# Kernel tuning notes

Hardware: AMD Instinct MI355X
Metric: run time of the kernel (lower is better)

## Reference

```python
import jax, jax.numpy as jnp
import numpy as np

NUM_LABELS = 32
EMB = 128          # label_embedding_dim
HID = 1024         # hidden_dim (== encoder feature dim)
B, S = 128, 512


def setup_inputs() -> dict:
    key = jax.random.key(0)
    ks = jax.random.split(key, 8)
    k = 1.0 / np.sqrt(HID)  # torch GRU/Linear default init bound
    u = lambda kk, shape: jax.random.uniform(kk, shape, jnp.float32, minval=-k, maxval=k)
    return {
        "hidden_states": jax.random.normal(ks[0], (B, S, HID), jnp.float32),
        "emb": jax.random.normal(ks[1], (NUM_LABELS, EMB), jnp.float32),  # nn.Embedding ~ N(0,1)
        "W_ih": u(ks[2], (3 * HID, EMB + HID)),  # GRU input weights, gate order r,z,n
        "W_hh": u(ks[3], (3 * HID, HID)),
        "b_ih": u(ks[4], (3 * HID,)),
        "b_hh": u(ks[5], (3 * HID,)),
        "W_out": u(ks[6], (NUM_LABELS, HID)),
        "b_out": u(ks[7], (NUM_LABELS,)),
    }


def reference(hidden_states, emb, W_ih, W_hh, b_ih, b_hh, W_out, b_out):
    batch = hidden_states.shape[0]
    h0 = jnp.zeros((batch, W_hh.shape[1]), hidden_states.dtype)
    lab0 = jnp.broadcast_to(emb[0], (batch, emb.shape[1]))  # label_start_embedding (id 0)

    def step(carry, x_t):
        h, lab = carry
        inp = jnp.concatenate([x_t, lab], axis=-1)            # [B, HID+EMB]
        gi = inp @ W_ih.T + b_ih                               # [B, 3*HID]
        gh = h @ W_hh.T + b_hh
        ir, iz, in_ = jnp.split(gi, 3, axis=-1)
        hr, hz, hn = jnp.split(gh, 3, axis=-1)
        r = jax.nn.sigmoid(ir + hr)
        z = jax.nn.sigmoid(iz + hz)
        n = jnp.tanh(in_ + r * hn)
        h_new = (1.0 - z) * n + z * h                          # PyTorch GRU update
        logit = h_new @ W_out.T + b_out                        # dropout is identity in eval
        pred = jnp.argmax(logit, axis=-1)                      # softmax is monotone; argmax(probs)==argmax(logit)
        return (h_new, emb[pred]), logit

    xs = jnp.swapaxes(hidden_states, 0, 1)                     # [S, B, HID]
    _, logits = jax.lax.scan(step, (h0, lab0), xs)             # logits: [S, B, L]
    return jnp.swapaxes(logits, 0, 1)                          # [B, S, L]
```

## Files before the change

### kernel.cpp

```cpp
#include <hip/hip_runtime.h>


#define S_    512
#define HID_  1024
#define EMB_  128
#define NL_   32
#define G3_   3072

#define LDS_A_STRIDE 1032
#define LDS_A_BYTES  (48 * LDS_A_STRIDE * 2)
#define CP_STRIDE    52
#define LDS_CP_BYTES (4 * 64 * CP_STRIDE * 4)
#define LDS_BYTES    (LDS_A_BYTES + LDS_CP_BYTES)

typedef __attribute__((ext_vector_type(8))) short          short8;
typedef __attribute__((ext_vector_type(8))) unsigned short u16x8;
typedef __attribute__((ext_vector_type(4))) unsigned short u16x4;
typedef __attribute__((ext_vector_type(4))) float          f32x4;
typedef unsigned long long u64_t;

__device__ unsigned int   g_ctr[576];
__device__ unsigned int   g_flag[1];
__device__ unsigned int   g_vis[256];
__device__ unsigned int   g_predflag;
__device__ int            g_pred[128];
__device__ unsigned short g_hhi[2][128 * HID_];
__device__ unsigned short g_hlo[2][128 * HID_];
__device__ float          g_hf32[2][128 * HID_];
__device__ float          g_Glab[NL_ * G3_];
__device__ unsigned short g_Wlox[G3_ * HID_];
__device__ unsigned short g_Wlohh[G3_ * HID_];
__device__ float          g_GIXall[(size_t)S_ * 128 * 64 * 48];

__device__ __forceinline__ float bf2f(unsigned short u) {
  union { unsigned int i; float f; } v; v.i = ((unsigned int)u) << 16; return v.f;
}
__device__ __forceinline__ unsigned short f2bf(float f) {
  union { float f; unsigned int i; } v; v.f = f;
  unsigned int u = v.i;
  return (unsigned short)((u + 0x7FFFu + ((u >> 16) & 1u)) >> 16);
}
__device__ __forceinline__ short8 ld_bf8(const unsigned short* p) {
  return __builtin_bit_cast(short8, *(const u16x8*)p);
}
__device__ __forceinline__ float ldin(const void* p, long i, int f32) {
  return f32 ? ((const float*)p)[i] : bf2f(((const unsigned short*)p)[i]);
}
__device__ __forceinline__ void store_out(void* out, int f32, long idx, float v) {
  if (f32) ((float*)out)[idx] = v;
  else     ((unsigned short*)out)[idx] = f2bf(v);
}

__device__ __forceinline__ u64_t ald64(const void* p) {
  return __hip_atomic_load((const u64_t*)p, __ATOMIC_RELAXED,
                           __HIP_MEMORY_SCOPE_AGENT);
}
__device__ __forceinline__ void ast64(void* p, u64_t v) {
  __hip_atomic_store((u64_t*)p, v, __ATOMIC_RELAXED,
                     __HIP_MEMORY_SCOPE_AGENT);
}
__device__ __forceinline__ unsigned int ald32(const unsigned int* p) {
  return __hip_atomic_load(p, __ATOMIC_RELAXED, __HIP_MEMORY_SCOPE_AGENT);
}
__device__ __forceinline__ void ast32(unsigned int* p, unsigned int v) {
  __hip_atomic_store(p, v, __ATOMIC_RELAXED, __HIP_MEMORY_SCOPE_AGENT);
}
__device__ __forceinline__ int aldi(const int* p) {
  return __hip_atomic_load(p, __ATOMIC_RELAXED, __HIP_MEMORY_SCOPE_AGENT);
}
__device__ __forceinline__ void asti(int* p, int v) {
  __hip_atomic_store(p, v, __ATOMIC_RELAXED, __HIP_MEMORY_SCOPE_AGENT);
}
__device__ __forceinline__ short8 ld_bf8_coh(const unsigned short* p) {
  union { u64_t q[2]; short8 s; } u;
  u.q[0] = ald64(p);
  u.q[1] = ald64(p + 4);
  return u.s;
}
__device__ __forceinline__ f32x4 ld_f4_coh(const float* p) {
  union { u64_t q[2]; f32x4 f; } u;
  u.q[0] = ald64(p);
  u.q[1] = ald64(p + 2);
  return u.f;
}
__device__ __forceinline__ void st_f4_coh(float* p, f32x4 v) {
  union { f32x4 f; u64_t q[2]; } u; u.f = v;
  ast64(p, u.q[0]);
  ast64(p + 2, u.q[1]);
}
__device__ __forceinline__ void st_h4_coh(unsigned short* p, u16x4 v) {
  union { u16x4 h; u64_t q; } u; u.h = v;
  ast64(p, u.q);
}

__global__ void k_zero() {
  int t = blockIdx.x * 256 + threadIdx.x;
  if (t < 576) g_ctr[t] = 0u;
  else if (t < 832) g_vis[t - 576] = 0u;
  else if (t < 960) g_pred[t - 832] = 0;
  else if (t == 960) g_predflag = 0u;
  const u16x4 z4 = {0, 0, 0, 0};
  const f32x4 zf = {0.f, 0.f, 0.f, 0.f};
  for (int i = t; i < 2 * 128 * HID_ / 4; i += 65536) {
    ((u16x4*)g_hhi)[i] = z4;
    ((u16x4*)g_hlo)[i] = z4;
    ((f32x4*)g_hf32)[i] = zf;
  }
}

__global__ void k_detect(const unsigned short* __restrict__ W) {
  unsigned bad = 0;
  for (int i = threadIdx.x; i < 1024; i += 64) {
    float v = bf2f(W[i]);
    if (!(v * v <= 1.0f)) bad = 1;
  }
  unsigned long long b = __ballot(bad != 0);
  if (threadIdx.x == 0) g_flag[0] = (b != 0ull) ? 1u : 0u;
}

__global__ void k_prep(const void* __restrict__ emb,
                       const void* __restrict__ W_ih,
                       const void* __restrict__ b_ih) {
  const int f32 = (int)g_flag[0];
  int l = blockIdx.x / 12;
  int n = (blockIdx.x % 12) * 256 + threadIdx.x;
  double acc = (double)ldin(b_ih, n, f32);
  for (int e = 0; e < EMB_; ++e)
    acc += (double)ldin(emb, (long)l * EMB_ + e, f32) *
           (double)ldin(W_ih, (long)n * (HID_ + EMB_) + HID_ + e, f32);
  g_Glab[l * G3_ + n] = (float)acc;
}

__global__ void k_prepw(const void* __restrict__ W_ih,
                        const void* __restrict__ W_hh) {
  if (!g_flag[0]) return;
  long i4 = ((long)blockIdx.x * 256 + threadIdx.x) * 4;
  if (i4 >= (long)G3_ * HID_) return;
  int row = (int)(i4 >> 10), col = (int)(i4 & 1023);
  f32x4 wh = *(const f32x4*)&((const float*)W_hh)[(long)row * HID_ + col];
  f32x4 wx = *(const f32x4*)&((const float*)W_ih)[(long)row * (HID_ + EMB_) + col];
  u16x4 lh, lx;
  #pragma unroll
  for (int j = 0; j < 4; ++j) {
    unsigned short h1 = f2bf(wh[j]);
    lh[j] = f2bf(wh[j] - bf2f(h1));
    unsigned short x1 = f2bf(wx[j]);
    lx[j] = f2bf(wx[j] - bf2f(x1));
  }
  *(u16x4*)&g_Wlohh[i4] = lh;
  *(u16x4*)&g_Wlox[i4]  = lx;
}

__device__ __forceinline__ void gridbar(int wg, int bar) {
  __syncthreads();
  if (threadIdx.x == 0) {
    asm volatile("s_waitcnt vmcnt(0)" ::: "memory");
    unsigned int* c1   = g_ctr + (wg & 7) * 64;
    unsigned int* root = g_ctr + 512;
    unsigned int old = __hip_atomic_fetch_add(c1, 1u, __ATOMIC_RELAXED,
                                              __HIP_MEMORY_SCOPE_AGENT);
    if (old == 32u * (unsigned)(bar + 1) - 1u)
      __hip_atomic_fetch_add(root, 1u, __ATOMIC_RELAXED,
                             __HIP_MEMORY_SCOPE_AGENT);
    unsigned int tgt = 8u * (unsigned)(bar + 1);
    while (__hip_atomic_load(root, __ATOMIC_RELAXED,
                             __HIP_MEMORY_SCOPE_AGENT) < tgt)
      __builtin_amdgcn_s_sleep(1);
  }
  __syncthreads();
}

__device__ __forceinline__ void stage_w(unsigned short* sA, const void* Wsrc,
                                        int wstride, int rg, int f32, int tid) {
  if (f32) {
    const float* Ws = (const float*)Wsrc;
    for (int i = tid; i < 48 * 1024 / 4; i += 256) {
      int e = i * 4, row = e >> 10, k4 = e & 1023;
      int grow = (row >> 4) * HID_ + rg * 16 + (row & 15);
      f32x4 v = *(const f32x4*)&Ws[(long)grow * wstride + k4];
      u16x4 o;
      #pragma unroll
      for (int j = 0; j < 4; ++j) o[j] = f2bf(v[j]);
      *(u16x4*)&sA[row * LDS_A_STRIDE + k4] = o;
    }
  } else {
    const unsigned short* Ws = (const unsigned short*)Wsrc;
    for (int i = tid; i < 48 * 1024 / 4; i += 256) {
      int e = i * 4, row = e >> 10, k4 = e & 1023;
      int grow = (row >> 4) * HID_ + rg * 16 + (row & 15);
      *(u16x4*)&sA[row * LDS_A_STRIDE + k4] =
          *(const u16x4*)&Ws[(long)grow * wstride + k4];
    }
  }
}

__global__ __launch_bounds__(256) void k_seq(
    const void* __restrict__ hs,
    const void* __restrict__ W_ih,
    const void* __restrict__ W_hh,
    const void* __restrict__ b_hh,
    const void* __restrict__ W_out,
    const void* __restrict__ b_out,
    void* __restrict__ out) {
  extern __shared__ char smem[];
  unsigned short* sA  = (unsigned short*)smem;
  float*          sCp = (float*)(smem + LDS_A_BYTES);

  const int f32 = (int)g_flag[0];
  const int tid = threadIdx.x;
  const int wg  = blockIdx.x;
  const bool isx = (wg < 128);
  const int lid  = isx ? wg : wg - 128;
  const int rg = lid >> 1, bg = lid & 1;
  const int slot = lid;
  const int lane = tid & 63, wv = tid >> 6;
  const int m = lane & 15, q = lane >> 4;
  const int bl = tid & 63;
  const int jj = (tid >> 6) * 4;
  const int kw0 = wv * 256 + q * 8;

  int bar = 0;

  if (tid == 0) ast32(&g_vis[wg], (unsigned)wg + 1u);
  gridbar(wg, bar); ++bar;
  if (tid == 0) {
    unsigned p = ((unsigned)wg + 37u) & 255u;
    if (ald32(&g_vis[p]) != p + 1u) store_out(out, f32, wg, 999.0f);
  }

  {
    const int slot0 = wg & 127;
    const int rg0 = slot0 >> 1, bg0 = slot0 & 1;
    stage_w(sA, W_ih, HID_ + EMB_, rg0, f32, tid);
    __syncthreads();
    const long bstride = (long)S_ * HID_;
    const long boffb = (long)(bg0 * 64) * S_ * HID_;
    for (int t = 0; t < 256; ++t) {
      const int it = ((wg >> 7) << 8) | t;
      f32x4 acc[3][4];
      #pragma unroll
      for (int rt = 0; rt < 3; ++rt)
        #pragma unroll
        for (int bt = 0; bt < 4; ++bt) acc[rt][bt] = f32x4{0.f, 0.f, 0.f, 0.f};
      const long boff = boffb + (long)it * HID_;
      if (f32) {
        const float* Bf = (const float*)hs + boff;
        #pragma unroll
        for (int kb = 0; kb < 8; ++kb) {
          const int k = kw0 + kb * 32;
          short8 avh[3];
          #pragma unroll
          for (int rt = 0; rt < 3; ++rt)
            avh[rt] = ld_bf8(&sA[(rt * 16 + m) * LDS_A_STRIDE + k]);
          short8 bxh[4], bxl[4];
          #pragma unroll
          for (int bt = 0; bt < 4; ++bt) {
            const float* bp = Bf + (long)(bt * 16 + m) * bstride + k;
            f32x4 x0 = *(const f32x4*)bp;
            f32x4 x1 = *(const f32x4*)(bp + 4);
            u16x8 th, tl;
            #pragma unroll
            for (int j = 0; j < 4; ++j) {
              unsigned short u0 = f2bf(x0[j]);
              th[j] = u0; tl[j] = f2bf(x0[j] - bf2f(u0));
              unsigned short u1 = f2bf(x1[j]);
              th[4 + j] = u1; tl[4 + j] = f2bf(x1[j] - bf2f(u1));
            }
            bxh[bt] = __builtin_bit_cast(short8, th);
            bxl[bt] = __builtin_bit_cast(short8, tl);
          }
          short8 avl[3];
          #pragma unroll
          for (int rt = 0; rt < 3; ++rt)
            avl[rt] = ld_bf8(&g_Wlox[(long)(rt * HID_ + rg0 * 16 + m) * HID_ + k]);
          #pragma unroll
          for (int rt = 0; rt < 3; ++rt)
            #pragma unroll
            for (int bt = 0; bt < 4; ++bt) {
              acc[rt][bt] = __builtin_amdgcn_mfma_f32_16x16x32_bf16(
                  avh[rt], bxh[bt], acc[rt][bt], 0, 0, 0);
              acc[rt][bt] = __builtin_amdgcn_mfma_f32_16x16x32_bf16(
                  avh[rt], bxl[bt], acc[rt][bt], 0, 0, 0);
              acc[rt][bt] = __builtin_amdgcn_mfma_f32_16x16x32_bf16(
                  avl[rt], bxh[bt], acc[rt][bt], 0, 0, 0);
              acc[rt][bt] = __builtin_amdgcn_mfma_f32_16x16x32_bf16(
                  avl[rt], bxl[bt], acc[rt][bt], 0, 0, 0);
            }
        }
      } else {
        const unsigned short* Bh = (const unsigned short*)hs + boff;
        #pragma unroll
        for (int kb = 0; kb < 8; ++kb) {
          const int k = kw0 + kb * 32;
          short8 avh[3], bxh[4];
          #pragma unroll
          for (int rt = 0; rt < 3; ++rt)
            avh[rt] = ld_bf8(&sA[(rt * 16 + m) * LDS_A_STRIDE + k]);
          #pragma unroll
          for (int bt = 0; bt < 4; ++bt)
            bxh[bt] = ld_bf8(&Bh[(long)(bt * 16 + m) * bstride + k]);
          #pragma unroll
          for (int rt = 0; rt < 3; ++rt)
            #pragma unroll
            for (int bt = 0; bt < 4; ++bt)
              acc[rt][bt] = __builtin_amdgcn_mfma_f32_16x16x32_bf16(
                  avh[rt], bxh[bt], acc[rt][bt], 0, 0, 0);
        }
      }
      __syncthreads();
      #pragma unroll
      for (int rt = 0; rt < 3; ++rt)
        #pragma unroll
        for (int bt = 0; bt < 4; ++bt)
          *(f32x4*)&sCp[(wv * 64 + bt * 16 + m) * CP_STRIDE + rt * 16 + q * 4] =
              acc[rt][bt];
      __syncthreads();
      #pragma unroll
      for (int g = 0; g < 3; ++g) {
        f32x4 sv = f32x4{0.f, 0.f, 0.f, 0.f};
        #pragma unroll
        for (int w = 0; w < 4; ++w)
          sv += *(const f32x4*)&sCp[(w * 64 + bl) * CP_STRIDE + g * 16 + jj];
        *(f32x4*)&g_GIXall[(((long)it * 128 + slot0) * 64 + bl) * 48 +
                           g * 16 + jj] = sv;
      }
      __syncthreads();
    }
  }
  __threadfence();
  gridbar(wg, bar); ++bar;

  if (!isx) stage_w(sA, W_hh, HID_, rg, f32, tid);
  __syncthreads();

  float bo = 0.f;
  if (isx && tid < 32) bo = ldin(b_out, tid, f32);
  f32x4 bhh[3];
  if (!isx) {
    const int jbase = rg * 16 + jj;
    #pragma unroll
    for (int g = 0; g < 3; ++g)
      #pragma unroll
      for (int t = 0; t < 4; ++t)
        bhh[g][t] = ldin(b_hh, (long)g * HID_ + jbase + t, f32);
  }

  float hreg[4] = {0.f, 0.f, 0.f, 0.f};
  f32x4 sred[3];

  for (int it = 0; it <= S_; ++it) {
    gridbar(wg, bar); ++bar;

    if (isx && it >= 1) {
      const int rb = (it + 1) & 1;
      if (it == 1 && wg == 0 && tid == 0) {
        float s = 0.f;
        for (int i = 0; i < 16; ++i) {
          union { u64_t q; float f[2]; } u; u.q = ald64(&g_hf32[0][2 * i]);
          s += u.f[0] * u.f[0] + u.f[1] * u.f[1];
        }
        if (s == 0.f) store_out(out, f32, 300, 555.0f);
      }
      const int b = wg, s = it - 1;
      float* scrp  = sCp;
      float* shrow = sCp + 256;
      {
        f32x4 hv = ld_f4_coh(&g_hf32[rb][(long)b * HID_ + tid * 4]);
        *(f32x4*)&shrow[(tid >> 5) * 132 + (tid & 31) * 4] = hv;
      }
      __syncthreads();
      {
        int l = tid >> 3, kc = tid & 7;
        const float* hr = shrow + kc * 132;
        float p = 0.f;
        if (f32) {
          const float* wr = (const float*)W_out + (long)l * HID_ + kc * 128;
          for (int k = 0; k < 128; k += 4) {
            f32x4 wa = *(const f32x4*)&wr[k];
            f32x4 ha = *(const f32x4*)&hr[k];
            #pragma unroll
            for (int j = 0; j < 4; ++j) p += wa[j] * ha[j];
          }
        } else {
          const unsigned short* wr =
              (const unsigned short*)W_out + (long)l * HID_ + kc * 128;
          for (int k = 0; k < 128; k += 8) {
            u16x8 w8 = *(const u16x8*)&wr[k];
            f32x4 ha = *(const f32x4*)&hr[k];
            f32x4 hb = *(const f32x4*)&hr[k + 4];
            #pragma unroll
            for (int j = 0; j < 4; ++j) {
              p += bf2f(w8[j]) * ha[j];
              p += bf2f(w8[4 + j]) * hb[j];
            }
          }
        }
        scrp[tid] = p;
      }
      __syncthreads();
      if (tid < 32) {
        const float* pp = sCp + tid * 8;
        float v = pp[0] + pp[1] + pp[2] + pp[3] + pp[4] + pp[5] + pp[6] + pp[7]
                  + bo;
        store_out(out, f32, ((long)b * S_ + s) * NL_ + tid, v);
        float bv = v; int bi = tid;
        #pragma unroll
        for (int off = 16; off; off >>= 1) {
          float v2 = __shfl_down(bv, off, 32);
          int   i2 = __shfl_down(bi, off, 32);
          if (v2 > bv || (v2 == bv && i2 < bi)) { bv = v2; bi = i2; }
        }
        if (tid == 0) {
          asti(&g_pred[b], bi);
          asm volatile("s_waitcnt vmcnt(0)" ::: "memory");
          __hip_atomic_fetch_add(&g_predflag, 1u, __ATOMIC_RELAXED,
                                 __HIP_MEMORY_SCOPE_AGENT);
        }
      }
      __syncthreads();
    }

    if (!isx && it < S_) {
      const int rb = (it + 1) & 1;
      const int wb = it & 1;
      f32x4 gixp[3];
      #pragma unroll
      for (int g = 0; g < 3; ++g)
        gixp[g] = *(const f32x4*)&g_GIXall[(((long)it * 128 + slot) * 64 + bl)
                                           * 48 + g * 16 + jj];

      f32x4 acc[3][4];
      #pragma unroll
      for (int rt = 0; rt < 3; ++rt)
        #pragma unroll
        for (int bt = 0; bt < 4; ++bt) acc[rt][bt] = f32x4{0.f, 0.f, 0.f, 0.f};

      const unsigned short* Bhi = g_hhi[rb] + (long)(bg * 64) * HID_;
      const unsigned short* Blo = g_hlo[rb] + (long)(bg * 64) * HID_;
      #pragma unroll
      for (int kb = 0; kb < 8; ++kb) {
        const int k = kw0 + kb * 32;
        short8 avh[3], bh[4], blv[4];
        #pragma unroll
        for (int rt = 0; rt < 3; ++rt)
          avh[rt] = ld_bf8(&sA[(rt * 16 + m) * LDS_A_STRIDE + k]);
        #pragma unroll
        for (int bt = 0; bt < 4; ++bt) {
          bh[bt]  = ld_bf8_coh(&Bhi[(long)(bt * 16 + m) * HID_ + k]);
          blv[bt] = ld_bf8_coh(&Blo[(long)(bt * 16 + m) * HID_ + k]);
        }
        #pragma unroll
        for (int rt = 0; rt < 3; ++rt)
          #pragma unroll
          for (int bt = 0; bt < 4; ++bt) {
            acc[rt][bt] = __builtin_amdgcn_mfma_f32_16x16x32_bf16(
                avh[rt], bh[bt], acc[rt][bt], 0, 0, 0);
            acc[rt][bt] = __builtin_amdgcn_mfma_f32_16x16x32_bf16(
                avh[rt], blv[bt], acc[rt][bt], 0, 0, 0);
          }
        if (f32) {
          short8 avl[3];
          #pragma unroll
          for (int rt = 0; rt < 3; ++rt)
            avl[rt] = ld_bf8(&g_Wlohh[(long)(rt * HID_ + rg * 16 + m) * HID_ + k]);
          #pragma unroll
          for (int rt = 0; rt < 3; ++rt)
            #pragma unroll
            for (int bt = 0; bt < 4; ++bt) {
              acc[rt][bt] = __builtin_amdgcn_mfma_f32_16x16x32_bf16(
                  avl[rt], bh[bt], acc[rt][bt], 0, 0, 0);
              acc[rt][bt] = __builtin_amdgcn_mfma_f32_16x16x32_bf16(
                  avl[rt], blv[bt], acc[rt][bt], 0, 0, 0);
            }
        }
      }

      __syncthreads();
      #pragma unroll
      for (int rt = 0; rt < 3; ++rt)
        #pragma unroll
        for (int bt = 0; bt < 4; ++bt)
          *(f32x4*)&sCp[(wv * 64 + bt * 16 + m) * CP_STRIDE + rt * 16 + q * 4] =
              acc[rt][bt];
      __syncthreads();
      #pragma unroll
      for (int g = 0; g < 3; ++g) {
        f32x4 sv = f32x4{0.f, 0.f, 0.f, 0.f};
        #pragma unroll
        for (int w = 0; w < 4; ++w)
          sv += *(const f32x4*)&sCp[(w * 64 + bl) * CP_STRIDE + g * 16 + jj];
        sred[g] = sv;
      }

      if (it >= 1) {
        if (tid == 0) {
          unsigned tgt = 128u * (unsigned)it;
          while (ald32(&g_predflag) < tgt) __builtin_amdgcn_s_sleep(1);
        }
        __syncthreads();
      }

      const int bglob = bg * 64 + bl;
      const int jbase = rg * 16 + jj;
      const int pb = aldi(&g_pred[bglob]);
      const float* gl = g_Glab + (long)pb * G3_;
      f32x4 glab[3];
      #pragma unroll
      for (int g = 0; g < 3; ++g)
        glab[g] = *(const f32x4*)&gl[g * HID_ + jbase];
      u16x4 whi, wlo;
      f32x4 hf;
      #pragma unroll
      for (int t4 = 0; t4 < 4; ++t4) {
        float ghr = sred[0][t4] + bhh[0][t4];
        float ghz = sred[1][t4] + bhh[1][t4];
        float ghn = sred[2][t4] + bhh[2][t4];
        float gir = gixp[0][t4] + glab[0][t4];
        float giz = gixp[1][t4] + glab[1][t4];
        float gin = gixp[2][t4] + glab[2][t4];
        float r = 1.f / (1.f + expf(-(gir + ghr)));
        float z = 1.f / (1.f + expf(-(giz + ghz)));
        float n = tanhf(gin + r * ghn);
        float hn = (1.f - z) * n + z * hreg[t4];
        hreg[t4] = hn;
        hf[t4] = hn;
        unsigned short uhi = f2bf(hn);
        whi[t4] = uhi;
        wlo[t4] = f2bf(hn - bf2f(uhi));
      }
      st_h4_coh(&g_hhi[wb][(long)bglob * HID_ + jbase], whi);
      st_h4_coh(&g_hlo[wb][(long)bglob * HID_ + jbase], wlo);
      st_f4_coh(&g_hf32[wb][(long)bglob * HID_ + jbase], hf);
    }
  }
}

extern "C" void kernel_launch(void* const* d_in, const int* in_sizes, int n_in,
                              void* d_out, int out_size, void* d_ws, size_t ws_size,
                              hipStream_t stream) {
  const void* hs    = d_in[0];
  const void* emb   = d_in[1];
  const void* W_ih  = d_in[2];
  const void* W_hh  = d_in[3];
  const void* b_ih  = d_in[4];
  const void* b_hh  = d_in[5];
  const void* W_out = d_in[6];
  const void* b_out = d_in[7];

  hipLaunchKernelGGL(k_zero, dim3(256), dim3(256), 0, stream);
  hipLaunchKernelGGL(k_detect, dim3(1), dim3(64), 0, stream,
                     (const unsigned short*)W_ih);
  hipLaunchKernelGGL(k_prep, dim3(32 * 12), dim3(256), 0, stream,
                     emb, W_ih, b_ih);
  hipLaunchKernelGGL(k_prepw, dim3(3072), dim3(256), 0, stream, W_ih, W_hh);
  hipFuncSetAttribute((const void*)k_seq,
                      hipFuncAttributeMaxDynamicSharedMemorySize, LDS_BYTES);
  hipLaunchKernelGGL(k_seq, dim3(256), dim3(256), LDS_BYTES, stream,
                     hs, W_ih, W_hh, b_hh, W_out, b_out, d_out);
}
```

Baseline: 17.38 ms.

## Replace per-step grid barrier with fine-grained sequence flags for h and predictions

Removes the full grid barrier each timestep. Hidden-state producers now publish per-row-group sequence counters (g_hseq), and consumers spin only on the 64 counters for their batch half. Predicted labels are packed with the step index into per-batch words, which replaces the global pred counter and removes a block-wide wait. This should cut barrier latency and let independent batch halves run ahead of each other. In exchange it relies on spin-waiting with relaxed atomics and careful ordering, which risks write-after-read hazards on the double-buffered h arrays now that no global barrier orders the steps.

```diff
diff --git a/kernel.cpp b/kernel.cpp
--- a/kernel.cpp
+++ b/kernel.cpp
@@ -22,8 +22,8 @@
 __device__ unsigned int   g_ctr[576];
 __device__ unsigned int   g_flag[1];
 __device__ unsigned int   g_vis[256];
-__device__ unsigned int   g_predflag;
-__device__ int            g_pred[128];
+__device__ unsigned int   g_hseq[2][64 * 16];
+__device__ unsigned int   g_predw[128 * 16];
 __device__ unsigned short g_hhi[2][128 * HID_];
 __device__ unsigned short g_hlo[2][128 * HID_];
 __device__ float          g_hf32[2][128 * HID_];
@@ -65,12 +65,6 @@
 __device__ __forceinline__ void ast32(unsigned int* p, unsigned int v) {
   __hip_atomic_store(p, v, __ATOMIC_RELAXED, __HIP_MEMORY_SCOPE_AGENT);
 }
-__device__ __forceinline__ int aldi(const int* p) {
-  return __hip_atomic_load(p, __ATOMIC_RELAXED, __HIP_MEMORY_SCOPE_AGENT);
-}
-__device__ __forceinline__ void asti(int* p, int v) {
-  __hip_atomic_store(p, v, __ATOMIC_RELAXED, __HIP_MEMORY_SCOPE_AGENT);
-}
 __device__ __forceinline__ short8 ld_bf8_coh(const unsigned short* p) {
   union { u64_t q[2]; short8 s; } u;
   u.q[0] = ald64(p);
@@ -97,8 +91,8 @@
   int t = blockIdx.x * 256 + threadIdx.x;
   if (t < 576) g_ctr[t] = 0u;
   else if (t < 832) g_vis[t - 576] = 0u;
-  else if (t < 960) g_pred[t - 832] = 0;
-  else if (t == 960) g_predflag = 0u;
+  if (t >= 2048 && t < 4096) ((unsigned int*)g_hseq)[t - 2048] = 0u;
+  if (t >= 4096 && t < 6144) g_predw[t - 4096] = 0u;
   const u16x4 z4 = {0, 0, 0, 0};
   const f32x4 zf = {0.f, 0.f, 0.f, 0.f};
   for (int i = t; i < 2 * 128 * HID_ / 4; i += 65536) {
@@ -167,6 +161,15 @@
                              __HIP_MEMORY_SCOPE_AGENT) < tgt)
       __builtin_amdgcn_s_sleep(1);
   }
+  __syncthreads();
+}
+
+__device__ __forceinline__ void wait_hseq(int half, int it) {
+  if (threadIdx.x < 64) {
+    const unsigned int* p = &g_hseq[half][threadIdx.x * 16];
+    while ((int)ald32(p) < it) { }
+  }
+  __builtin_amdgcn_sched_barrier(0);
   __syncthreads();
 }
 
@@ -349,9 +352,8 @@
   f32x4 sred[3];
 
   for (int it = 0; it <= S_; ++it) {
-    gridbar(wg, bar); ++bar;
-
     if (isx && it >= 1) {
+      wait_hseq(wg >> 6, it);
       const int rb = (it + 1) & 1;
       if (it == 1 && wg == 0 && tid == 0) {
         float s = 0.f;
@@ -410,24 +412,21 @@
           int   i2 = __shfl_down(bi, off, 32);
           if (v2 > bv || (v2 == bv && i2 < bi)) { bv = v2; bi = i2; }
         }
-        if (tid == 0) {
-          asti(&g_pred[b], bi);
-          asm volatile("s_waitcnt vmcnt(0)" ::: "memory");
-          __hip_atomic_fetch_add(&g_predflag, 1u, __ATOMIC_RELAXED,
-                                 __HIP_MEMORY_SCOPE_AGENT);
-        }
+        if (tid == 0) ast32(&g_predw[b * 16], ((unsigned)it << 8) | (unsigned)bi);
       }
       __syncthreads();
     }
 
     if (!isx && it < S_) {
-      const int rb = (it + 1) & 1;
-      const int wb = it & 1;
       f32x4 gixp[3];
       #pragma unroll
       for (int g = 0; g < 3; ++g)
         gixp[g] = *(const f32x4*)&g_GIXall[(((long)it * 128 + slot) * 64 + bl)
                                            * 48 + g * 16 + jj];
+
+      wait_hseq(bg, it);
+      const int rb = (it + 1) & 1;
+      const int wb = it & 1;
 
       f32x4 acc[3][4];
       #pragma unroll
@@ -492,17 +491,17 @@
         sred[g] = sv;
       }
 
+      const int bglob = bg * 64 + bl;
+      int pb = 0;
       if (it >= 1) {
-        if (tid == 0) {
-          unsigned tgt = 128u * (unsigned)it;
-          while (ald32(&g_predflag) < tgt) __builtin_amdgcn_s_sleep(1);
-        }
-        __syncthreads();
-      }
-
-      const int bglob = bg * 64 + bl;
+        const unsigned int* pw = &g_predw[bglob * 16];
+        unsigned w = ald32(pw);
+        while ((int)(w >> 8) < it) { w = ald32(pw); }
+        pb = (int)(w & 255u);
+      }
+      __builtin_amdgcn_sched_barrier(0);
+
       const int jbase = rg * 16 + jj;
-      const int pb = aldi(&g_pred[bglob]);
       const float* gl = g_Glab + (long)pb * G3_;
       f32x4 glab[3];
       #pragma unroll
@@ -531,6 +530,10 @@
       st_h4_coh(&g_hhi[wb][(long)bglob * HID_ + jbase], whi);
       st_h4_coh(&g_hlo[wb][(long)bglob * HID_ + jbase], wlo);
       st_f4_coh(&g_hf32[wb][(long)bglob * HID_ + jbase], hf);
+
+      asm volatile("s_waitcnt vmcnt(0)" ::: "memory");
+      __syncthreads();
+      if (tid == 0) ast32(&g_hseq[bg][rg * 16], (unsigned)(it + 1));
     }
   }
 }
```

After: 17.11 ms. Within noise of the previous version (-1.5%).
